# Performance work log

Measured on AMD Instinct MI355X. Metric: run time of the kernel, lower is better.

## Reference

```python
import jax, jax.numpy as jnp
import numpy as np

N, E, D, L, NE, FF, G, V, H = 4096, 131072, 256, 4, 2, 512, 128, 100, 8
DK = D // H


def setup_inputs() -> dict:
    key = jax.random.key(0)
    ks = iter(jax.random.split(key, 64))
    def W(shape, scale=0.05):
        return jax.random.normal(next(ks), shape, dtype=jnp.float32) * scale
    inp = {}
    inp['z'] = jax.random.randint(next(ks), (N,), 0, V)
    inp['pos'] = jax.random.normal(next(ks), (N, 3), dtype=jnp.float32)
    inp['batch'] = jnp.sort(jax.random.randint(next(ks), (N,), 0, G))
    inp['edge_index'] = jax.random.randint(next(ks), (2, E), 0, N)
    inp['emb'] = W((V, D))
    # E_GCL stacks (EGNN layer: edge MLP, attention gate, node MLP)
    inp['egcl_edge_w1'] = W((L, 2 * D + 1, D)); inp['egcl_edge_b1'] = jnp.zeros((L, D), jnp.float32)
    inp['egcl_edge_w2'] = W((L, D, D));         inp['egcl_edge_b2'] = jnp.zeros((L, D), jnp.float32)
    inp['egcl_node_w1'] = W((L, 2 * D, D));     inp['egcl_node_b1'] = jnp.zeros((L, D), jnp.float32)
    inp['egcl_node_w2'] = W((L, D, D));         inp['egcl_node_b2'] = jnp.zeros((L, D), jnp.float32)
    inp['egcl_att_w'] = W((L, D, 1));           inp['egcl_att_b'] = jnp.zeros((L, 1), jnp.float32)
    # Transformer encoder stacks (post-norm)
    inp['enc_wq'] = W((NE, D, D)); inp['enc_bq'] = jnp.zeros((NE, D), jnp.float32)
    inp['enc_wk'] = W((NE, D, D)); inp['enc_bk'] = jnp.zeros((NE, D), jnp.float32)
    inp['enc_wv'] = W((NE, D, D)); inp['enc_bv'] = jnp.zeros((NE, D), jnp.float32)
    inp['enc_wo'] = W((NE, D, D)); inp['enc_bo'] = jnp.zeros((NE, D), jnp.float32)
    inp['enc_ln1_g'] = jnp.ones((NE, D), jnp.float32); inp['enc_ln1_b'] = jnp.zeros((NE, D), jnp.float32)
    inp['enc_ffn_w1'] = W((NE, D, FF)); inp['enc_ffn_b1'] = jnp.zeros((NE, FF), jnp.float32)
    inp['enc_ffn_w2'] = W((NE, FF, D)); inp['enc_ffn_b2'] = jnp.zeros((NE, D), jnp.float32)
    inp['enc_ln2_g'] = jnp.ones((NE, D), jnp.float32); inp['enc_ln2_b'] = jnp.zeros((NE, D), jnp.float32)
    # energy_fc head
    inp['fc_w1'] = W((D, D)); inp['fc_b1'] = jnp.zeros((D,), jnp.float32)
    inp['fc_w2'] = W((D, 1)); inp['fc_b2'] = jnp.zeros((1,), jnp.float32)
    return inp


def _layer_norm(x, g, b, eps=1e-5):
    mu = jnp.mean(x, axis=-1, keepdims=True)
    var = jnp.mean((x - mu) ** 2, axis=-1, keepdims=True)
    return (x - mu) * jax.lax.rsqrt(var + eps) * g + b


def reference(z, pos, batch, edge_index, emb,
              egcl_edge_w1, egcl_edge_b1, egcl_edge_w2, egcl_edge_b2,
              egcl_node_w1, egcl_node_b1, egcl_node_w2, egcl_node_b2,
              egcl_att_w, egcl_att_b,
              enc_wq, enc_bq, enc_wk, enc_bk, enc_wv, enc_bv, enc_wo, enc_bo,
              enc_ln1_g, enc_ln1_b, enc_ffn_w1, enc_ffn_b1, enc_ffn_w2, enc_ffn_b2,
              enc_ln2_g, enc_ln2_b, fc_w1, fc_b1, fc_w2, fc_b2):
    h = emb[z]                                   # [N, D]
    row, col = edge_index[0], edge_index[1]
    diff = pos[row] - pos[col]                   # static_coord: coords never updated
    radial = jnp.sum(diff * diff, axis=-1, keepdims=True)  # [E, 1]
    for i in range(L):
        m_in = jnp.concatenate([h[row], h[col], radial], axis=-1)     # [E, 2D+1]
        m = jax.nn.silu(m_in @ egcl_edge_w1[i] + egcl_edge_b1[i])
        m = jax.nn.silu(m @ egcl_edge_w2[i] + egcl_edge_b2[i])        # [E, D]
        m = m * jax.nn.sigmoid(m @ egcl_att_w[i] + egcl_att_b[i])     # attention gate
        agg = jax.ops.segment_sum(m, row, num_segments=N)             # [N, D]
        n_in = jnp.concatenate([h, agg], axis=-1)
        upd = jax.nn.silu(n_in @ egcl_node_w1[i] + egcl_node_b1[i]) @ egcl_node_w2[i] + egcl_node_b2[i]
        h = h + upd                                                   # residual
    scale = 1.0 / jnp.sqrt(jnp.asarray(DK, h.dtype))
    for i in range(NE):
        q = (h @ enc_wq[i] + enc_bq[i]).reshape(N, H, DK)
        k = (h @ enc_wk[i] + enc_bk[i]).reshape(N, H, DK)
        v = (h @ enc_wv[i] + enc_bv[i]).reshape(N, H, DK)
        scores = jnp.einsum('nhd,mhd->hnm', q, k) * scale
        a = jax.nn.softmax(scores, axis=-1)
        attn = jnp.einsum('hnm,mhd->nhd', a, v).reshape(N, D) @ enc_wo[i] + enc_bo[i]
        h = _layer_norm(h + attn, enc_ln1_g[i], enc_ln1_b[i])
        f = jax.nn.silu(h @ enc_ffn_w1[i] + enc_ffn_b1[i]) @ enc_ffn_w2[i] + enc_ffn_b2[i]
        h = _layer_norm(h + f, enc_ln2_g[i], enc_ln2_b[i])
    g = jax.ops.segment_sum(h, batch, num_segments=G)                 # scatter-add readout
    out = jax.nn.silu(g @ fc_w1 + fc_b1) @ fc_w2 + fc_b2              # [G, 1]
    return out
```

## Files before the change

### kernel.cpp

```cpp
#include <hip/hip_runtime.h>
#include <math.h>

#define N_NODES 4096
#define N_EDGES 131072
#define DIM     256
#define NL      4
#define NENC    2
#define FFD     512
#define NG      128
#define NHEAD   8
#define DKH     32
#define TE2     32
#define NSPLIT_ATT 4

typedef __attribute__((ext_vector_type(8))) short bf16x8;
typedef __attribute__((ext_vector_type(4))) float f32x4;

__device__ __forceinline__ float siluf(float x) { return x / (1.f + __expf(-x)); }
__device__ __forceinline__ float sigmf_(float x) { return 1.f / (1.f + __expf(-x)); }
__device__ __forceinline__ unsigned short f2b(float f) {
    union { float f; unsigned u; } x; x.f = f;
    unsigned r = x.u + 0x7fffu + ((x.u >> 16) & 1u);
    return (unsigned short)(r >> 16);
}
__device__ __forceinline__ float b2f(unsigned short h) {
    union { unsigned u; float f; } x; x.u = (unsigned)h << 16; return x.f;
}

__global__ __launch_bounds__(256) void k_embed(const int* __restrict__ z,
                                               const float* __restrict__ emb,
                                               float* __restrict__ h) {
    int i = blockIdx.x * 256 + threadIdx.x;
    int n = i >> 8, d = i & 255;
    h[i] = emb[z[n] * DIM + d];
}

__global__ __launch_bounds__(256) void k_radial(const float* __restrict__ pos,
                                                const int* __restrict__ ei,
                                                float* __restrict__ radial) {
    int e = blockIdx.x * 256 + threadIdx.x;
    if (e >= N_EDGES) return;
    int r = ei[e], c = ei[N_EDGES + e];
    float dx = pos[r*3+0] - pos[c*3+0];
    float dy = pos[r*3+1] - pos[c*3+1];
    float dz = pos[r*3+2] - pos[c*3+2];
    radial[e] = dx*dx + dy*dy + dz*dz;
}

__global__ __launch_bounds__(256) void k_hist(const int* __restrict__ ei, int* __restrict__ cnt) {
    int e = blockIdx.x * 256 + threadIdx.x;
    if (e < N_EDGES) atomicAdd(&cnt[ei[e]], 1);
}

__global__ __launch_bounds__(256) void k_scan(const int* __restrict__ cnt, int* __restrict__ pos) {
    __shared__ int s_w[4];
    int t = threadIdx.x, lane = t & 63, wv = t >> 6;
    int loc[16]; int s = 0;
    #pragma unroll
    for (int i = 0; i < 16; ++i) { loc[i] = s; s += cnt[t * 16 + i]; }
    int inc = s;
    #pragma unroll
    for (int off = 1; off < 64; off <<= 1) {
        int v = __shfl_up(inc, off, 64);
        if (lane >= off) inc += v;
    }
    if (lane == 63) s_w[wv] = inc;
    __syncthreads();
    int wbase = 0;
    for (int j = 0; j < wv; ++j) wbase += s_w[j];
    int base = wbase + inc - s;
    #pragma unroll
    for (int i = 0; i < 16; ++i) pos[t * 16 + i] = base + loc[i];
}

__global__ __launch_bounds__(256) void k_scatter(const int* __restrict__ ei,
                                                 const float* __restrict__ radial,
                                                 int* __restrict__ pos,
                                                 int* __restrict__ rows_s,
                                                 int* __restrict__ cols_s,
                                                 float* __restrict__ rad_s) {
    int e = blockIdx.x * 256 + threadIdx.x;
    if (e >= N_EDGES) return;
    int r = ei[e];
    int p = atomicAdd(&pos[r], 1);
    rows_s[p] = r;
    cols_s[p] = ei[N_EDGES + e];
    rad_s[p] = radial[e];
}

__global__ __launch_bounds__(256) void k_conv_w2(const float* __restrict__ ew2,
                                                 unsigned short* __restrict__ W2F) {
    int tid = blockIdx.x * 256 + threadIdx.x;
    int layer = tid >> 13;
    int r = tid & 8191;
    int ks = r >> 10, ntg = (r >> 6) & 15, lane = r & 63;
    const float* W = ew2 + (size_t)layer * 65536;
    unsigned short tmp[8];
    #pragma unroll
    for (int j = 0; j < 8; ++j) {
        int k = ks*32 + 4*(lane>>4) + (j&3) + 16*(j>>2);
        int n = ntg*16 + (lane&15);
        tmp[j] = f2b(W[k*256 + n]);
    }
    *(bf16x8*)&W2F[(size_t)layer*65536 + (size_t)r*8] = *(const bf16x8*)&tmp[0];
}

__global__ __launch_bounds__(256) void k_pack_all(
    const float* __restrict__ ew1, const float* __restrict__ nw1, const float* __restrict__ nw2,
    const float* __restrict__ wq, const float* __restrict__ wk, const float* __restrict__ wv,
    const float* __restrict__ wo, const float* __restrict__ fw1, const float* __restrict__ fw2,
    unsigned short* __restrict__ dst)
{
    int f = blockIdx.x * 256 + threadIdx.x;
    int rem, panel, NTG, mode;
    if (f < 65536)       { rem = f;          panel = rem / 16384; rem &= 16383; NTG = 32; mode = 0; }
    else if (f < 131072) { rem = f - 65536;  panel = rem / 16384; rem &= 16383; NTG = 16; mode = 1; }
    else if (f < 163840) { rem = f - 131072; panel = rem / 8192;  rem &= 8191;  NTG = 16; mode = 2; }
    else if (f < 212992) { rem = f - 163840; panel = rem / 24576; rem %= 24576; NTG = 48; mode = 3; }
    else if (f < 229376) { rem = f - 212992; panel = rem / 8192;  rem &= 8191;  NTG = 16; mode = 4; }
    else if (f < 262144) { rem = f - 229376; panel = rem / 16384; rem &= 16383; NTG = 32; mode = 5; }
    else                 { rem = f - 262144; panel = rem / 16384; rem &= 16383; NTG = 16; mode = 6; }
    int ks   = rem / (NTG * 64);
    int ntg  = (rem >> 6) % NTG;
    int lane = rem & 63;
    unsigned short tmp[8];
    #pragma unroll
    for (int j = 0; j < 8; ++j) {
        int k = ks*32 + 4*(lane>>4) + (j&3) + 16*(j>>2);
        int n = ntg*16 + (lane&15);
        float val;
        switch (mode) {
            case 0: val = ew1[(size_t)panel*131328 + (n < 256 ? k*256 + n : (256 + k)*256 + (n - 256))]; break;
            case 1: val = nw1[(size_t)panel*131072 + k*256 + n]; break;
            case 2: val = nw2[(size_t)panel*65536 + k*256 + n]; break;
            case 3: { const float* b = (n < 256) ? wq : ((n < 512) ? wk : wv);
                      val = b[(size_t)panel*65536 + k*256 + (n & 255)]; } break;
            case 4: val = wo[(size_t)panel*65536 + k*256 + n]; break;
            case 5: val = fw1[(size_t)panel*131072 + k*512 + n]; break;
            default: val = fw2[(size_t)panel*131072 + k*256 + n]; break;
        }
        tmp[j] = f2b(val);
    }
    *(bf16x8*)&dst[(size_t)f * 8] = *(const bf16x8*)&tmp[0];
}

template<int NCHUNK, int NC, int NSPLIT, int ACT, int RESID, int OUTMODE>
__global__ __launch_bounds__(256) void k_gemm(
    const float* __restrict__ A0, const float* __restrict__ A1, int lda,
    const unsigned short* __restrict__ Wp,
    const float* __restrict__ b0, const float* __restrict__ b1, const float* __restrict__ b2,
    const float* __restrict__ resid, float* __restrict__ C,
    unsigned short* __restrict__ kpk, unsigned short* __restrict__ vpk)
{
    constexpr int NT  = NC / (64 * NSPLIT);
    constexpr int NTG = NC / 16;
    __shared__ __align__(16) char s_hi[16 * 512];
    __shared__ __align__(16) char s_lo[16 * 512];
    const int t = threadIdx.x, l = t & 63, w = t >> 6;
    const int g = l >> 4, r = l & 15;
    const int mtile  = blockIdx.x % 256;
    const int nchunk = blockIdx.x / 256;
    const int r0 = mtile * 16;

    f32x4 acc[NT];
    #pragma unroll
    for (int nt = 0; nt < NT; ++nt) acc[nt] = (f32x4){0.f, 0.f, 0.f, 0.f};

    const bf16x8* Wf = (const bf16x8*)Wp;
    for (int c = 0; c < NCHUNK; ++c) {
        const float* Ac = (c == 0) ? A0 : A1;
        __syncthreads();
        const int c4 = l * 4;
        #pragma unroll
        for (int it = 0; it < 4; ++it) {
            int row = it * 4 + w;
            float4 v = *(const float4*)&Ac[(size_t)(r0 + row) * lda + c4];
            float vv[4] = {v.x, v.y, v.z, v.w};
            ushort4 h4, l4;
            unsigned short hh;
            hh = f2b(vv[0]); h4.x = hh; l4.x = f2b(vv[0] - b2f(hh));
            hh = f2b(vv[1]); h4.y = hh; l4.y = f2b(vv[1] - b2f(hh));
            hh = f2b(vv[2]); h4.z = hh; l4.z = f2b(vv[2] - b2f(hh));
            hh = f2b(vv[3]); h4.w = hh; l4.w = f2b(vv[3] - b2f(hh));
            int boff = (c4 * 2) ^ (row << 3);
            *(ushort4*)&s_hi[row * 512 + boff] = h4;
            *(ushort4*)&s_lo[row * 512 + boff] = l4;
        }
        __syncthreads();
        #pragma unroll
        for (int ks = 0; ks < 8; ++ks) {
            const int ksg = c * 8 + ks;
            const int x0 = (ks * 64 + 8 * g) ^ (r << 3);
            union { uint2 u[2]; bf16x8 v; } ah, al;
            ah.u[0] = *(const uint2*)&s_hi[r * 512 + x0];
            ah.u[1] = *(const uint2*)&s_hi[r * 512 + (x0 ^ 32)];
            al.u[0] = *(const uint2*)&s_lo[r * 512 + x0];
            al.u[1] = *(const uint2*)&s_lo[r * 512 + (x0 ^ 32)];
            #pragma unroll
            for (int nt = 0; nt < NT; ++nt) {
                int fb = (nchunk * 4 + w) * NT + nt;
                bf16x8 bf_ = Wf[(size_t)(ksg * NTG + fb) * 64 + l];
                acc[nt] = __builtin_amdgcn_mfma_f32_16x16x32_bf16(ah.v, bf_, acc[nt], 0, 0, 0);
                acc[nt] = __builtin_amdgcn_mfma_f32_16x16x32_bf16(al.v, bf_, acc[nt], 0, 0, 0);
            }
        }
    }
    #pragma unroll
    for (int nt = 0; nt < NT; ++nt) {
        int n = ((nchunk * 4 + w) * NT + nt) * 16 + r;
        float bias = 0.f;
        if (b0) {
            const float* bp = (n < 256) ? b0 : ((n < 512) ? b1 : b2);
            bias = bp[n & 255];
        }
        #pragma unroll
        for (int reg = 0; reg < 4; ++reg) {
            int row = r0 + g * 4 + reg;
            float v = acc[nt][reg] + bias;
            if (ACT == 1) v = siluf(v);
            if (RESID) v += resid[(size_t)row * 256 + n];
            if (OUTMODE == 0) {
                C[(size_t)row * NC + n] = v;
            } else {
                if (n < 256) {
                    C[(size_t)row * 256 + n] = v;
                } else if (n < 512) {
                    int hd = (n - 256) >> 5, dm = (n - 256) & 31;
                    int dp = (dm & 3) | (((dm >> 4) & 1) << 2) | (((dm >> 2) & 3) << 3);
                    unsigned short hb = f2b(v);
                    size_t base = ((size_t)hd * N_NODES + row) * 64;
                    kpk[base + dp]      = hb;
                    kpk[base + 32 + dp] = f2b(v - b2f(hb));
                } else {
                    int hd = (n - 512) >> 5, dm = (n - 512) & 31;
                    int s = row & 31;
                    int sp = (s & 3) | (((s >> 4) & 1) << 2) | (((s >> 2) & 3) << 3);
                    int keyp = (row & ~31) | sp;
                    vpk[((size_t)hd * 32 + dm) * N_NODES + keyp] = f2b(v);
                }
            }
        }
    }
}

__global__ __launch_bounds__(256) void k_edge_mfma(
    const float* __restrict__ P12,
    const int* __restrict__ rows_s, const int* __restrict__ cols_s,
    const float* __restrict__ rad_s,
    const float* __restrict__ w1r, const float* __restrict__ b1,
    const unsigned short* __restrict__ W2F, const float* __restrict__ b2,
    const float* __restrict__ aw, const float* __restrict__ ab,
    float* __restrict__ agg)
{
    __shared__ __align__(16) char s_a[20480];
    __shared__ int   s_row[TE2], s_cn[TE2];
    __shared__ float s_rad[TE2], s_gp[4][TE2], s_gate[TE2];
    const int t = threadIdx.x, l = t & 63, w = t >> 6;
    const int e0 = blockIdx.x * TE2;

    if (t < TE2) {
        s_row[t] = rows_s[e0 + t];
        s_cn[t]  = cols_s[e0 + t];
        s_rad[t] = rad_s[e0 + t];
    }
    __syncthreads();

    const int c4 = l * 4;
    const float4 wr = *(const float4*)&w1r[c4];
    const float4 bb = *(const float4*)&b1[c4];
    #pragma unroll
    for (int it = 0; it < 8; ++it) {
        int e = it * 4 + w;
        float4 pa = *(const float4*)&P12[(size_t)s_row[e] * 512 + c4];
        float4 pb = *(const float4*)&P12[(size_t)s_cn[e] * 512 + 256 + c4];
        float rad = s_rad[e];
        ushort4 pk;
        pk.x = f2b(siluf(pa.x + pb.x + rad * wr.x + bb.x));
        pk.y = f2b(siluf(pa.y + pb.y + rad * wr.y + bb.y));
        pk.z = f2b(siluf(pa.z + pb.z + rad * wr.z + bb.z));
        pk.w = f2b(siluf(pa.w + pb.w + rad * wr.w + bb.w));
        *(ushort4*)&s_a[e * 512 + ((c4 * 2) ^ ((e & 15) << 3))] = pk;
    }
    __syncthreads();

    const int g = l >> 4, r = l & 15;
    f32x4 acc[2][4];
    #pragma unroll
    for (int mt = 0; mt < 2; ++mt)
        #pragma unroll
        for (int nt = 0; nt < 4; ++nt)
            acc[mt][nt] = (f32x4){0.f, 0.f, 0.f, 0.f};

    const bf16x8* Wf = (const bf16x8*)W2F;
    for (int ks = 0; ks < 8; ++ks) {
        bf16x8 af[2], bfr[4];
        #pragma unroll
        for (int mt = 0; mt < 2; ++mt) {
            int rowa = mt * 16 + r;
            int x0 = (ks * 64 + 8 * g) ^ (r << 3);
            uint2 lo = *(const uint2*)&s_a[rowa * 512 + x0];
            uint2 hi = *(const uint2*)&s_a[rowa * 512 + (x0 ^ 32)];
            union { uint2 u[2]; bf16x8 v; } ua;
            ua.u[0] = lo; ua.u[1] = hi;
            af[mt] = ua.v;
        }
        #pragma unroll
        for (int nt = 0; nt < 4; ++nt)
            bfr[nt] = Wf[(ks * 16 + w * 4 + nt) * 64 + l];
        #pragma unroll
        for (int mt = 0; mt < 2; ++mt)
            #pragma unroll
            for (int nt = 0; nt < 4; ++nt)
                acc[mt][nt] = __builtin_amdgcn_mfma_f32_16x16x32_bf16(af[mt], bfr[nt], acc[mt][nt], 0, 0, 0);
    }

    float b2v[4], awv[4];
    #pragma unroll
    for (int nt = 0; nt < 4; ++nt) {
        int col = w * 64 + nt * 16 + r;
        b2v[nt] = b2[col];
        awv[nt] = aw[col];
    }
    float pg[2][4];
    #pragma unroll
    for (int mt = 0; mt < 2; ++mt)
        #pragma unroll
        for (int reg = 0; reg < 4; ++reg) {
            float s = 0.f;
            #pragma unroll
            for (int nt = 0; nt < 4; ++nt) {
                float v = siluf(acc[mt][nt][reg] + b2v[nt]);
                acc[mt][nt][reg] = v;
                s += v * awv[nt];
            }
            pg[mt][reg] = s;
        }
    #pragma unroll
    for (int off = 1; off < 16; off <<= 1)
        #pragma unroll
        for (int mt = 0; mt < 2; ++mt)
            #pragma unroll
            for (int reg = 0; reg < 4; ++reg)
                pg[mt][reg] += __shfl_xor(pg[mt][reg], off, 64);
    if (r == 0) {
        #pragma unroll
        for (int mt = 0; mt < 2; ++mt)
            #pragma unroll
            for (int reg = 0; reg < 4; ++reg)
                s_gp[w][mt * 16 + g * 4 + reg] = pg[mt][reg];
    }
    __syncthreads();
    if (t < TE2)
        s_gate[t] = sigmf_(s_gp[0][t] + s_gp[1][t] + s_gp[2][t] + s_gp[3][t] + ab[0]);
    __syncthreads();

    unsigned short* s_out = (unsigned short*)s_a;
    #pragma unroll
    for (int mt = 0; mt < 2; ++mt) {
        float4 gt4 = *(const float4*)&s_gate[mt * 16 + g * 4];
        #pragma unroll
        for (int nt = 0; nt < 4; ++nt) {
            int col = w * 64 + nt * 16 + r;
            ushort4 o4;
            o4.x = f2b(acc[mt][nt][0] * gt4.x);
            o4.y = f2b(acc[mt][nt][1] * gt4.y);
            o4.z = f2b(acc[mt][nt][2] * gt4.z);
            o4.w = f2b(acc[mt][nt][3] * gt4.w);
            *(ushort4*)&s_out[col * 40 + mt * 16 + g * 4] = o4;
        }
    }
    __syncthreads();
    float cur = 0.f;
    #pragma unroll
    for (int c = 0; c < 4; ++c) {
        union { uint4 q; unsigned short s[8]; } ch;
        ch.q = *(const uint4*)&s_out[t * 40 + c * 8];
        #pragma unroll
        for (int j = 0; j < 8; ++j) {
            int e = c * 8 + j;
            cur += b2f(ch.s[j]);
            bool flush = (e == TE2 - 1) || (s_row[e + 1] != s_row[e]);
            if (flush) {
                atomicAdd(&agg[(size_t)s_row[e] * DIM + t], cur);
                cur = 0.f;
            }
        }
    }
}

template<int ACT>
__global__ __launch_bounds__(256) void k_mlp_small(
    const float* __restrict__ A1, const float* __restrict__ W,
    const float* __restrict__ bias, float* __restrict__ C)
{
    __shared__ float s_a[16][260];
    const int t  = threadIdx.x;
    const int r0 = blockIdx.x * 16;
    for (int r = 0; r < 16; ++r)
        s_a[r][t] = A1[(size_t)(r0 + r) * DIM + t];
    __syncthreads();
    const int er0 = (t >> 6) * 4;
    const int c0 = (t & 63) * 4;
    float acc[4][4];
    #pragma unroll
    for (int e = 0; e < 4; ++e)
        #pragma unroll
        for (int c = 0; c < 4; ++c) acc[e][c] = 0.f;
    #pragma unroll 2
    for (int k = 0; k < DIM; k += 4) {
        float4 w0 = *(const float4*)&W[(size_t)(k+0)*DIM + c0];
        float4 w1 = *(const float4*)&W[(size_t)(k+1)*DIM + c0];
        float4 w2 = *(const float4*)&W[(size_t)(k+2)*DIM + c0];
        float4 w3 = *(const float4*)&W[(size_t)(k+3)*DIM + c0];
        #pragma unroll
        for (int e = 0; e < 4; ++e) {
            float4 x = *(const float4*)&s_a[er0+e][k];
            acc[e][0] += x.x*w0.x + x.y*w1.x + x.z*w2.x + x.w*w3.x;
            acc[e][1] += x.x*w0.y + x.y*w1.y + x.z*w2.y + x.w*w3.y;
            acc[e][2] += x.x*w0.z + x.y*w1.z + x.z*w2.z + x.w*w3.z;
            acc[e][3] += x.x*w0.w + x.y*w1.w + x.z*w2.w + x.w*w3.w;
        }
    }
    float4 bb = *(const float4*)&bias[c0];
    #pragma unroll
    for (int e = 0; e < 4; ++e) {
        float v0 = acc[e][0] + bb.x, v1 = acc[e][1] + bb.y;
        float v2 = acc[e][2] + bb.z, v3 = acc[e][3] + bb.w;
        if (ACT == 1) { v0 = siluf(v0); v1 = siluf(v1); v2 = siluf(v2); v3 = siluf(v3); }
        float4 o; o.x = v0; o.y = v1; o.z = v2; o.w = v3;
        *(float4*)&C[(size_t)(r0 + er0 + e) * DIM + c0] = o;
    }
}

__global__ __launch_bounds__(256) void k_ln(const float* __restrict__ x,
                                            const float* __restrict__ g,
                                            const float* __restrict__ b,
                                            float* __restrict__ out) {
    int t = threadIdx.x, lane = t & 63, w = t >> 6;
    int row = blockIdx.x * 4 + w;
    float4 v = *(const float4*)&x[(size_t)row * DIM + lane * 4];
    float s = v.x + v.y + v.z + v.w;
    #pragma unroll
    for (int off = 32; off; off >>= 1) s += __shfl_xor(s, off, 64);
    float mu = s * (1.f / 256.f);
    float dx = v.x - mu, dy = v.y - mu, dz = v.z - mu, dw = v.w - mu;
    float q = dx*dx + dy*dy + dz*dz + dw*dw;
    #pragma unroll
    for (int off = 32; off; off >>= 1) q += __shfl_xor(q, off, 64);
    float rs = rsqrtf(q * (1.f / 256.f) + 1e-5f);
    float4 gg = *(const float4*)&g[lane * 4];
    float4 bb = *(const float4*)&b[lane * 4];
    float4 o;
    o.x = dx * rs * gg.x + bb.x;
    o.y = dy * rs * gg.y + bb.y;
    o.z = dz * rs * gg.z + bb.z;
    o.w = dw * rs * gg.w + bb.w;
    *(float4*)&out[(size_t)row * DIM + lane * 4] = o;
}

__global__ __launch_bounds__(256) void k_attn_mfma(
    const float* __restrict__ q,
    const unsigned short* __restrict__ kpk,
    const unsigned short* __restrict__ vpk,
    float* __restrict__ op0, float* __restrict__ op1,
    float* __restrict__ op2, float* __restrict__ op3,
    float* __restrict__ mlbuf)
{
    __shared__ __align__(16) char s_k[2][8192];
    __shared__ __align__(16) char s_v[2][4096];
    const int t = threadIdx.x, lane = t & 63, w = t >> 6;
    const int g = lane >> 4, r = lane & 15;
    const int head = blockIdx.y;
    const int split = blockIdx.z;
    const int q0 = blockIdx.x * 64;
    const float scale = 0.17677669529663687f;

    bf16x8 qh, ql;
    {
        const float* qp = &q[(size_t)(q0 + w*16 + r) * DIM + head*DKH + 4*g];
        float4 f0 = *(const float4*)qp;
        float4 f1 = *(const float4*)(qp + 16);
        float vv[8] = {f0.x, f0.y, f0.z, f0.w, f1.x, f1.y, f1.z, f1.w};
        union { unsigned short s[8]; bf16x8 v; } uh, ul;
        #pragma unroll
        for (int j = 0; j < 8; ++j) {
            float sv = vv[j] * scale;
            unsigned short hb = f2b(sv);
            uh.s[j] = hb;
            ul.s[j] = f2b(sv - b2f(hb));
        }
        qh = uh.v; ql = ul.v;
    }

    const char* kbase = (const char*)(kpk + (size_t)head * N_NODES * 64) + (size_t)split * 16 * 8192;
    const unsigned short* vbase = vpk + (size_t)head * 32 * N_NODES;
    const int koff = split * 1024;
    const int vrow = t >> 3, vch = t & 7;

    uint4 kr0, kr1, vr0;
    {
        const char* kt = kbase;
        kr0 = *(const uint4*)(kt + t * 16);
        kr1 = *(const uint4*)(kt + 4096 + t * 16);
        vr0 = *(const uint4*)(vbase + (size_t)vrow * N_NODES + koff + vch * 8);
        int key0 = t >> 3, sl0 = t & 7;
        *(uint4*)&s_k[0][key0 * 128 + ((sl0 ^ (key0 & 7)) << 4)] = kr0;
        int c1 = t + 256, key1 = c1 >> 3, sl1 = c1 & 7;
        *(uint4*)&s_k[0][key1 * 128 + ((sl1 ^ (key1 & 7)) << 4)] = kr1;
        *(uint4*)&s_v[0][vrow * 128 + ((vch ^ (vrow & 7)) << 4)] = vr0;
    }
    __syncthreads();

    float m = -1e30f, l = 0.f;
    f32x4 ot0 = (f32x4){0.f,0.f,0.f,0.f}, ot1 = (f32x4){0.f,0.f,0.f,0.f};

    for (int tile = 0; tile < 16; ++tile) {
        const int cur = tile & 1;
        if (tile < 15) {
            const char* kt = kbase + (size_t)(tile + 1) * 8192;
            kr0 = *(const uint4*)(kt + t * 16);
            kr1 = *(const uint4*)(kt + 4096 + t * 16);
            vr0 = *(const uint4*)(vbase + (size_t)vrow * N_NODES + koff + (tile + 1) * 64 + vch * 8);
        }
        bf16x8 kh[4], kl[4];
        #pragma unroll
        for (int kb = 0; kb < 4; ++kb) {
            int key = kb * 16 + r;
            kh[kb] = *(const bf16x8*)&s_k[cur][key * 128 + ((g ^ (r & 7)) << 4)];
            kl[kb] = *(const bf16x8*)&s_k[cur][key * 128 + (((4 + g) ^ (r & 7)) << 4)];
        }
        f32x4 sc[4];
        #pragma unroll
        for (int kb = 0; kb < 4; ++kb) {
            f32x4 a = (f32x4){0.f,0.f,0.f,0.f};
            a = __builtin_amdgcn_mfma_f32_16x16x32_bf16(kh[kb], qh, a, 0, 0, 0);
            a = __builtin_amdgcn_mfma_f32_16x16x32_bf16(kh[kb], ql, a, 0, 0, 0);
            a = __builtin_amdgcn_mfma_f32_16x16x32_bf16(kl[kb], qh, a, 0, 0, 0);
            sc[kb] = a;
        }
        float tm = -1e30f;
        #pragma unroll
        for (int kb = 0; kb < 4; ++kb)
            #pragma unroll
            for (int e = 0; e < 4; ++e) tm = fmaxf(tm, sc[kb][e]);
        tm = fmaxf(tm, __shfl_xor(tm, 16, 64));
        tm = fmaxf(tm, __shfl_xor(tm, 32, 64));
        float nm = fmaxf(m, tm);
        float scf = __expf(m - nm);
        m = nm;
        float p[16]; float ls = 0.f;
        #pragma unroll
        for (int kb = 0; kb < 4; ++kb)
            #pragma unroll
            for (int e = 0; e < 4; ++e) {
                float pe = __expf(sc[kb][e] - nm);
                p[kb*4+e] = pe; ls += pe;
            }
        ls += __shfl_xor(ls, 16, 64);
        ls += __shfl_xor(ls, 32, 64);
        l = l * scf + ls;
        ot0[0] *= scf; ot0[1] *= scf; ot0[2] *= scf; ot0[3] *= scf;
        ot1[0] *= scf; ot1[1] *= scf; ot1[2] *= scf; ot1[3] *= scf;
        union { unsigned short s[8]; bf16x8 v; } pk0, pk1;
        #pragma unroll
        for (int j = 0; j < 8; ++j) {
            pk0.s[j] = f2b(p[(j >> 2) * 4 + (j & 3)]);
            pk1.s[j] = f2b(p[(2 + (j >> 2)) * 4 + (j & 3)]);
        }
        bf16x8 vf00 = *(const bf16x8*)&s_v[cur][(0*16 + r) * 128 + (((0*4 + g) ^ (r & 7)) << 4)];
        bf16x8 vf01 = *(const bf16x8*)&s_v[cur][(0*16 + r) * 128 + (((1*4 + g) ^ (r & 7)) << 4)];
        bf16x8 vf10 = *(const bf16x8*)&s_v[cur][(1*16 + r) * 128 + (((0*4 + g) ^ (r & 7)) << 4)];
        bf16x8 vf11 = *(const bf16x8*)&s_v[cur][(1*16 + r) * 128 + (((1*4 + g) ^ (r & 7)) << 4)];
        ot0 = __builtin_amdgcn_mfma_f32_16x16x32_bf16(vf00, pk0.v, ot0, 0, 0, 0);
        ot0 = __builtin_amdgcn_mfma_f32_16x16x32_bf16(vf01, pk1.v, ot0, 0, 0, 0);
        ot1 = __builtin_amdgcn_mfma_f32_16x16x32_bf16(vf10, pk0.v, ot1, 0, 0, 0);
        ot1 = __builtin_amdgcn_mfma_f32_16x16x32_bf16(vf11, pk1.v, ot1, 0, 0, 0);

        __syncthreads();
        if (tile < 15) {
            int key0 = t >> 3, sl0 = t & 7;
            *(uint4*)&s_k[cur ^ 1][key0 * 128 + ((sl0 ^ (key0 & 7)) << 4)] = kr0;
            int c1 = t + 256, key1 = c1 >> 3, sl1 = c1 & 7;
            *(uint4*)&s_k[cur ^ 1][key1 * 128 + ((sl1 ^ (key1 & 7)) << 4)] = kr1;
            *(uint4*)&s_v[cur ^ 1][vrow * 128 + ((vch ^ (vrow & 7)) << 4)] = vr0;
        }
        __syncthreads();
    }

    float* opsel = (split == 0) ? op0 : (split == 1) ? op1 : (split == 2) ? op2 : op3;
    float* op = opsel + (size_t)(q0 + w*16 + r) * DIM + head*DKH;
    *(float4*)(op + 4*g)      = make_float4(ot0[0], ot0[1], ot0[2], ot0[3]);
    *(float4*)(op + 16 + 4*g) = make_float4(ot1[0], ot1[1], ot1[2], ot1[3]);
    if (g == 0) {
        float* mp = &mlbuf[(((size_t)split * NHEAD + head) * N_NODES + q0 + w*16 + r) * 2];
        mp[0] = m; mp[1] = l;
    }
}

__global__ __launch_bounds__(256) void k_attn_merge(
    const float* __restrict__ o0, const float* __restrict__ o1,
    const float* __restrict__ o2, const float* __restrict__ o3,
    const float* __restrict__ ml, float* __restrict__ A)
{
    int i = blockIdx.x * 256 + threadIdx.x;
    int qq = (i * 4) >> 8;
    int head = ((i * 4) & 255) >> 5;
    float m_[4], l_[4];
    #pragma unroll
    for (int s = 0; s < 4; ++s) {
        const float* p = &ml[(((size_t)s * NHEAD + head) * N_NODES + qq) * 2];
        m_[s] = p[0]; l_[s] = p[1];
    }
    float mm = fmaxf(fmaxf(m_[0], m_[1]), fmaxf(m_[2], m_[3]));
    float e0 = __expf(m_[0] - mm), e1 = __expf(m_[1] - mm);
    float e2 = __expf(m_[2] - mm), e3 = __expf(m_[3] - mm);
    float inv = 1.f / (e0 * l_[0] + e1 * l_[1] + e2 * l_[2] + e3 * l_[3]);
    float4 a0 = ((const float4*)o0)[i];
    float4 a1 = ((const float4*)o1)[i];
    float4 a2 = ((const float4*)o2)[i];
    float4 a3 = ((const float4*)o3)[i];
    float4 o;
    o.x = (a0.x*e0 + a1.x*e1 + a2.x*e2 + a3.x*e3) * inv;
    o.y = (a0.y*e0 + a1.y*e1 + a2.y*e2 + a3.y*e3) * inv;
    o.z = (a0.z*e0 + a1.z*e1 + a2.z*e2 + a3.z*e3) * inv;
    o.w = (a0.w*e0 + a1.w*e1 + a2.w*e2 + a3.w*e3) * inv;
    ((float4*)A)[i] = o;
}

__global__ __launch_bounds__(256) void k_segsum(const float* __restrict__ h,
                                                const int* __restrict__ batch,
                                                float* __restrict__ gbuf) {
    int i = blockIdx.x * 256 + threadIdx.x;
    int n = i >> 8, d = i & 255;
    atomicAdd(&gbuf[batch[n] * DIM + d], h[i]);
}

__global__ __launch_bounds__(256) void k_head2(const float* __restrict__ gmid,
                                               const float* __restrict__ w2,
                                               const float* __restrict__ b2,
                                               float* __restrict__ out) {
    int t = threadIdx.x, lane = t & 63, w = t >> 6;
    int g = blockIdx.x * 4 + w;
    float4 x  = *(const float4*)&gmid[g * DIM + lane * 4];
    float4 ww = *(const float4*)&w2[lane * 4];
    float s = x.x * ww.x + x.y * ww.y + x.z * ww.z + x.w * ww.w;
    #pragma unroll
    for (int off = 32; off; off >>= 1) s += __shfl_xor(s, off, 64);
    if (lane == 0) out[g] = s + b2[0];
}

extern "C" void kernel_launch(void* const* d_in, const int* in_sizes, int n_in,
                              void* d_out, int out_size, void* d_ws, size_t ws_size,
                              hipStream_t stream)
{
    const int*   z     = (const int*)d_in[0];
    const float* pos   = (const float*)d_in[1];
    const int*   batch = (const int*)d_in[2];
    const int*   ei    = (const int*)d_in[3];
    const float* emb   = (const float*)d_in[4];
    const float* ew1   = (const float*)d_in[5];
    const float* eb1   = (const float*)d_in[6];
    const float* ew2   = (const float*)d_in[7];
    const float* eb2   = (const float*)d_in[8];
    const float* nw1   = (const float*)d_in[9];
    const float* nb1   = (const float*)d_in[10];
    const float* nw2   = (const float*)d_in[11];
    const float* nb2   = (const float*)d_in[12];
    const float* aw    = (const float*)d_in[13];
    const float* ab    = (const float*)d_in[14];
    const float* wq    = (const float*)d_in[15];
    const float* bq    = (const float*)d_in[16];
    const float* wk    = (const float*)d_in[17];
    const float* bk    = (const float*)d_in[18];
    const float* wv    = (const float*)d_in[19];
    const float* bv    = (const float*)d_in[20];
    const float* wo    = (const float*)d_in[21];
    const float* bo    = (const float*)d_in[22];
    const float* ln1g  = (const float*)d_in[23];
    const float* ln1b  = (const float*)d_in[24];
    const float* fw1   = (const float*)d_in[25];
    const float* fb1   = (const float*)d_in[26];
    const float* fw2   = (const float*)d_in[27];
    const float* fb2   = (const float*)d_in[28];
    const float* ln2g  = (const float*)d_in[29];
    const float* ln2b  = (const float*)d_in[30];
    const float* fcw1  = (const float*)d_in[31];
    const float* fcb1  = (const float*)d_in[32];
    const float* fcw2  = (const float*)d_in[33];
    const float* fcb2  = (const float*)d_in[34];
    float* out = (float*)d_out;

    float* ws = (float*)d_ws;
    const size_t ND = (size_t)N_NODES * DIM;
    float* h    = ws;
    float* agg  = ws + ND;
    float* A    = ws + 2 * ND;
    float* U    = ws + 3 * ND;
    float* op0  = ws + 4 * ND;
    float* op1  = ws + 5 * ND;
    float* Bffn = ws + 6 * ND;
    unsigned short* kpk = (unsigned short*)Bffn;
    unsigned short* vpk = kpk + (size_t)NHEAD * N_NODES * 64;
    float* radial = Bffn + (3 * ND) / 2;
    int*   cnt    = (int*)(radial + N_EDGES);
    int*   pcur   = cnt + N_NODES;
    float* gbuf   = ws + 8 * ND;
    float* gmid   = gbuf + (size_t)NG * DIM;
    float* rad_s  = gmid + (size_t)NG * DIM;
    int*   rows_s = (int*)(rad_s + N_EDGES);
    int*   cols_s = rows_s + N_EDGES;
    unsigned short* W2F   = (unsigned short*)(cols_s + N_EDGES);
    unsigned short* packs = W2F + (size_t)NL * 65536;
    float* mlbuf = rad_s;

    unsigned short* PK_W1   = packs;
    unsigned short* PK_NW1  = packs + 524288;
    unsigned short* PK_NW2  = packs + 1048576;
    unsigned short* PK_QKV  = packs + 1310720;
    unsigned short* PK_WO   = packs + 1703936;
    unsigned short* PK_FFN1 = packs + 1835008;
    unsigned short* PK_FFN2 = packs + 2097152;

    dim3 b256(256);

    k_embed<<<N_NODES * DIM / 256, b256, 0, stream>>>(z, emb, h);
    k_radial<<<N_EDGES / 256, b256, 0, stream>>>(pos, ei, radial);
    k_conv_w2<<<NL * 8192 / 256, b256, 0, stream>>>(ew2, W2F);
    k_pack_all<<<1152, b256, 0, stream>>>(ew1, nw1, nw2, wq, wk, wv, wo, fw1, fw2, packs);

    hipMemsetAsync(cnt, 0, N_NODES * sizeof(int), stream);
    k_hist<<<N_EDGES / 256, b256, 0, stream>>>(ei, cnt);
    k_scan<<<1, b256, 0, stream>>>(cnt, pcur);
    k_scatter<<<N_EDGES / 256, b256, 0, stream>>>(ei, radial, pcur, rows_s, cols_s, rad_s);

    for (int l = 0; l < NL; ++l) {
        hipMemsetAsync(agg, 0, ND * sizeof(float), stream);
        const float* W1l = ew1 + (size_t)l * 513 * DIM;
        k_gemm<1,512,2,0,0,0><<<512, b256, 0, stream>>>(h, nullptr, DIM,
            PK_W1 + (size_t)l * 131072, nullptr, nullptr, nullptr, nullptr, U,
            nullptr, nullptr);
        k_edge_mfma<<<N_EDGES / TE2, b256, 0, stream>>>(U, rows_s, cols_s, rad_s,
            W1l + (size_t)512 * DIM, eb1 + (size_t)l * DIM,
            W2F + (size_t)l * 65536, eb2 + (size_t)l * DIM,
            aw + (size_t)l * DIM, ab + l, agg);
        const float* nb1l = nb1 + (size_t)l * DIM;
        k_gemm<2,256,2,1,0,0><<<512, b256, 0, stream>>>(h, agg, DIM,
            PK_NW1 + (size_t)l * 131072, nb1l, nb1l, nb1l, nullptr, A,
            nullptr, nullptr);
        const float* nb2l = nb2 + (size_t)l * DIM;
        k_gemm<1,256,2,0,1,0><<<512, b256, 0, stream>>>(A, nullptr, DIM,
            PK_NW2 + (size_t)l * 65536, nb2l, nb2l, nb2l, h, h,
            nullptr, nullptr);
    }

    for (int i = 0; i < NENC; ++i) {
        k_gemm<1,768,3,0,0,1><<<768, b256, 0, stream>>>(h, nullptr, DIM,
            PK_QKV + (size_t)i * 196608,
            bq + (size_t)i * DIM, bk + (size_t)i * DIM, bv + (size_t)i * DIM, nullptr, U,
            kpk, vpk);
        dim3 ag(N_NODES / 64, NHEAD, NSPLIT_ATT);
        k_attn_mfma<<<ag, b256, 0, stream>>>(U, kpk, vpk, op0, op1, A, agg, mlbuf);
        k_attn_merge<<<N_NODES * DIM / 1024, b256, 0, stream>>>(op0, op1, A, agg, mlbuf, A);
        const float* bol = bo + (size_t)i * DIM;
        k_gemm<1,256,2,0,1,0><<<512, b256, 0, stream>>>(A, nullptr, DIM,
            PK_WO + (size_t)i * 65536, bol, bol, bol, h, agg,
            nullptr, nullptr);
        k_ln<<<N_NODES / 4, b256, 0, stream>>>(agg, ln1g + (size_t)i * DIM, ln1b + (size_t)i * DIM, h);
        const float* fb1l = fb1 + (size_t)i * FFD;
        k_gemm<1,512,2,1,0,0><<<512, b256, 0, stream>>>(h, nullptr, DIM,
            PK_FFN1 + (size_t)i * 131072, fb1l, fb1l + 256, nullptr, nullptr, Bffn,
            nullptr, nullptr);
        const float* fb2l = fb2 + (size_t)i * DIM;
        k_gemm<2,256,2,0,1,0><<<512, b256, 0, stream>>>(Bffn, Bffn + 256, FFD,
            PK_FFN2 + (size_t)i * 131072, fb2l, fb2l, fb2l, h, agg,
            nullptr, nullptr);
        k_ln<<<N_NODES / 4, b256, 0, stream>>>(agg, ln2g + (size_t)i * DIM, ln2b + (size_t)i * DIM, h);
    }

    hipMemsetAsync(gbuf, 0, (size_t)NG * DIM * sizeof(float), stream);
    k_segsum<<<N_NODES * DIM / 256, b256, 0, stream>>>(h, batch, gbuf);
    k_mlp_small<1><<<NG / 16, b256, 0, stream>>>(gbuf, fcw1, fcb1, gmid);
    k_head2<<<NG / 4, b256, 0, stream>>>(gmid, fcw2, fcb2, out);
}
```

Baseline: 668.0 us.

## Fuse split-attention merge into Wo GEMM A-load and use uniform edge indices

Removes the separate k_attn_merge kernel. The four split-softmax partial outputs are now combined with their max/sum statistics inside the Wo projection GEMM's A-tile load. The fourth partial buffer moves from agg to a new op3buf region carved out after the packed weights. The edge kernel also precomputes the segment-flush mask with a ballot and uses readfirstlane to make row, column and radial values scalar-uniform, which cuts LDS reads and divergence in the atomic flush loop. The cost is extra exp and load work per GEMM tile, repeated across column-split blocks, and the added buffer must fit within the existing workspace.

```diff
diff --git a/kernel.cpp b/kernel.cpp
--- a/kernel.cpp
+++ b/kernel.cpp
@@ -144,13 +144,15 @@
     *(bf16x8*)&dst[(size_t)f * 8] = *(const bf16x8*)&tmp[0];
 }
 
-template<int NCHUNK, int NC, int NSPLIT, int ACT, int RESID, int OUTMODE>
+template<int NCHUNK, int NC, int NSPLIT, int ACT, int RESID, int OUTMODE, int AMODE>
 __global__ __launch_bounds__(256) void k_gemm(
     const float* __restrict__ A0, const float* __restrict__ A1, int lda,
     const unsigned short* __restrict__ Wp,
     const float* __restrict__ b0, const float* __restrict__ b1, const float* __restrict__ b2,
     const float* __restrict__ resid, float* __restrict__ C,
-    unsigned short* __restrict__ kpk, unsigned short* __restrict__ vpk)
+    unsigned short* __restrict__ kpk, unsigned short* __restrict__ vpk,
+    const float* __restrict__ am2, const float* __restrict__ am3,
+    const float* __restrict__ aml)
 {
     constexpr int NT  = NC / (64 * NSPLIT);
     constexpr int NTG = NC / 16;
@@ -174,7 +176,31 @@
         #pragma unroll
         for (int it = 0; it < 4; ++it) {
             int row = it * 4 + w;
-            float4 v = *(const float4*)&Ac[(size_t)(r0 + row) * lda + c4];
+            float4 v;
+            if (AMODE == 0) {
+                v = *(const float4*)&Ac[(size_t)(r0 + row) * lda + c4];
+            } else {
+                const int head = l >> 3;
+                float m_[4], l_[4];
+                #pragma unroll
+                for (int s = 0; s < 4; ++s) {
+                    const float* p = &aml[(((size_t)s * NHEAD + head) * N_NODES + (r0 + row)) * 2];
+                    m_[s] = p[0]; l_[s] = p[1];
+                }
+                float mm = fmaxf(fmaxf(m_[0], m_[1]), fmaxf(m_[2], m_[3]));
+                float e0 = __expf(m_[0] - mm), e1 = __expf(m_[1] - mm);
+                float e2 = __expf(m_[2] - mm), e3 = __expf(m_[3] - mm);
+                float inv = 1.f / (e0 * l_[0] + e1 * l_[1] + e2 * l_[2] + e3 * l_[3]);
+                size_t off = (size_t)(r0 + row) * 256 + c4;
+                float4 a0 = *(const float4*)&A0[off];
+                float4 a1 = *(const float4*)&A1[off];
+                float4 a2 = *(const float4*)&am2[off];
+                float4 a3 = *(const float4*)&am3[off];
+                v.x = (a0.x*e0 + a1.x*e1 + a2.x*e2 + a3.x*e3) * inv;
+                v.y = (a0.y*e0 + a1.y*e1 + a2.y*e2 + a3.y*e3) * inv;
+                v.z = (a0.z*e0 + a1.z*e1 + a2.z*e2 + a3.z*e3) * inv;
+                v.w = (a0.w*e0 + a1.w*e1 + a2.w*e2 + a3.w*e3) * inv;
+            }
             float vv[4] = {v.x, v.y, v.z, v.w};
             ushort4 h4, l4;
             unsigned short hh;
@@ -255,6 +281,7 @@
     __shared__ __align__(16) char s_a[20480];
     __shared__ int   s_row[TE2], s_cn[TE2];
     __shared__ float s_rad[TE2], s_gp[4][TE2], s_gate[TE2];
+    __shared__ unsigned s_mask;
     const int t = threadIdx.x, l = t & 63, w = t >> 6;
     const int e0 = blockIdx.x * TE2;
 
@@ -265,15 +292,23 @@
     }
     __syncthreads();
 
+    if (t < 64) {
+        bool flag = (t < TE2) && ((t == TE2 - 1) || (s_row[t + 1] != s_row[t]));
+        unsigned long long bm = __ballot(flag);
+        if (t == 0) s_mask = (unsigned)bm;
+    }
+
     const int c4 = l * 4;
     const float4 wr = *(const float4*)&w1r[c4];
     const float4 bb = *(const float4*)&b1[c4];
     #pragma unroll
     for (int it = 0; it < 8; ++it) {
         int e = it * 4 + w;
-        float4 pa = *(const float4*)&P12[(size_t)s_row[e] * 512 + c4];
-        float4 pb = *(const float4*)&P12[(size_t)s_cn[e] * 512 + 256 + c4];
-        float rad = s_rad[e];
+        int rowu = __builtin_amdgcn_readfirstlane(s_row[e]);
+        int cnu  = __builtin_amdgcn_readfirstlane(s_cn[e]);
+        float rad = __int_as_float(__builtin_amdgcn_readfirstlane(__float_as_int(s_rad[e])));
+        float4 pa = *(const float4*)&P12[(size_t)rowu * 512 + c4];
+        float4 pb = *(const float4*)&P12[(size_t)cnu * 512 + 256 + c4];
         ushort4 pk;
         pk.x = f2b(siluf(pa.x + pb.x + rad * wr.x + bb.x));
         pk.y = f2b(siluf(pa.y + pb.y + rad * wr.y + bb.y));
@@ -370,6 +405,7 @@
         }
     }
     __syncthreads();
+    const unsigned fmask = s_mask;
     float cur = 0.f;
     #pragma unroll
     for (int c = 0; c < 4; ++c) {
@@ -379,9 +415,9 @@
         for (int j = 0; j < 8; ++j) {
             int e = c * 8 + j;
             cur += b2f(ch.s[j]);
-            bool flush = (e == TE2 - 1) || (s_row[e + 1] != s_row[e]);
-            if (flush) {
-                atomicAdd(&agg[(size_t)s_row[e] * DIM + t], cur);
+            if ((fmask >> e) & 1u) {
+                int rowu = __builtin_amdgcn_readfirstlane(s_row[e]);
+                atomicAdd(&agg[(size_t)rowu * DIM + t], cur);
                 cur = 0.f;
             }
         }
@@ -595,36 +631,6 @@
         float* mp = &mlbuf[(((size_t)split * NHEAD + head) * N_NODES + q0 + w*16 + r) * 2];
         mp[0] = m; mp[1] = l;
     }
-}
-
-__global__ __launch_bounds__(256) void k_attn_merge(
-    const float* __restrict__ o0, const float* __restrict__ o1,
-    const float* __restrict__ o2, const float* __restrict__ o3,
-    const float* __restrict__ ml, float* __restrict__ A)
-{
-    int i = blockIdx.x * 256 + threadIdx.x;
-    int qq = (i * 4) >> 8;
-    int head = ((i * 4) & 255) >> 5;
-    float m_[4], l_[4];
-    #pragma unroll
-    for (int s = 0; s < 4; ++s) {
-        const float* p = &ml[(((size_t)s * NHEAD + head) * N_NODES + qq) * 2];
-        m_[s] = p[0]; l_[s] = p[1];
-    }
-    float mm = fmaxf(fmaxf(m_[0], m_[1]), fmaxf(m_[2], m_[3]));
-    float e0 = __expf(m_[0] - mm), e1 = __expf(m_[1] - mm);
-    float e2 = __expf(m_[2] - mm), e3 = __expf(m_[3] - mm);
-    float inv = 1.f / (e0 * l_[0] + e1 * l_[1] + e2 * l_[2] + e3 * l_[3]);
-    float4 a0 = ((const float4*)o0)[i];
-    float4 a1 = ((const float4*)o1)[i];
-    float4 a2 = ((const float4*)o2)[i];
-    float4 a3 = ((const float4*)o3)[i];
-    float4 o;
-    o.x = (a0.x*e0 + a1.x*e1 + a2.x*e2 + a3.x*e3) * inv;
-    o.y = (a0.y*e0 + a1.y*e1 + a2.y*e2 + a3.y*e3) * inv;
-    o.z = (a0.z*e0 + a1.z*e1 + a2.z*e2 + a3.z*e3) * inv;
-    o.w = (a0.w*e0 + a1.w*e1 + a2.w*e2 + a3.w*e3) * inv;
-    ((float4*)A)[i] = o;
 }
 
 __global__ __launch_bounds__(256) void k_segsum(const float* __restrict__ h,
@@ -712,6 +718,7 @@
     unsigned short* W2F   = (unsigned short*)(cols_s + N_EDGES);
     unsigned short* packs = W2F + (size_t)NL * 65536;
     float* mlbuf = rad_s;
+    float* op3buf = (float*)(packs + 2359296);
 
     unsigned short* PK_W1   = packs;
     unsigned short* PK_NW1  = packs + 524288;
@@ -736,44 +743,43 @@
     for (int l = 0; l < NL; ++l) {
         hipMemsetAsync(agg, 0, ND * sizeof(float), stream);
         const float* W1l = ew1 + (size_t)l * 513 * DIM;
-        k_gemm<1,512,2,0,0,0><<<512, b256, 0, stream>>>(h, nullptr, DIM,
+        k_gemm<1,512,2,0,0,0,0><<<512, b256, 0, stream>>>(h, nullptr, DIM,
             PK_W1 + (size_t)l * 131072, nullptr, nullptr, nullptr, nullptr, U,
-            nullptr, nullptr);
+            nullptr, nullptr, nullptr, nullptr, nullptr);
         k_edge_mfma<<<N_EDGES / TE2, b256, 0, stream>>>(U, rows_s, cols_s, rad_s,
             W1l + (size_t)512 * DIM, eb1 + (size_t)l * DIM,
             W2F + (size_t)l * 65536, eb2 + (size_t)l * DIM,
             aw + (size_t)l * DIM, ab + l, agg);
         const float* nb1l = nb1 + (size_t)l * DIM;
-        k_gemm<2,256,2,1,0,0><<<512, b256, 0, stream>>>(h, agg, DIM,
+        k_gemm<2,256,2,1,0,0,0><<<512, b256, 0, stream>>>(h, agg, DIM,
             PK_NW1 + (size_t)l * 131072, nb1l, nb1l, nb1l, nullptr, A,
-            nullptr, nullptr);
+            nullptr, nullptr, nullptr, nullptr, nullptr);
         const float* nb2l = nb2 + (size_t)l * DIM;
-        k_gemm<1,256,2,0,1,0><<<512, b256, 0, stream>>>(A, nullptr, DIM,
+        k_gemm<1,256,2,0,1,0,0><<<512, b256, 0, stream>>>(A, nullptr, DIM,
             PK_NW2 + (size_t)l * 65536, nb2l, nb2l, nb2l, h, h,
-            nullptr, nullptr);
+            nullptr, nullptr, nullptr, nullptr, nullptr);
     }
 
     for (int i = 0; i < NENC; ++i) {
-        k_gemm<1,768,3,0,0,1><<<768, b256, 0, stream>>>(h, nullptr, DIM,
+        k_gemm<1,768,3,0,0,1,0><<<768, b256, 0, stream>>>(h, nullptr, DIM,
             PK_QKV + (size_t)i * 196608,
             bq + (size_t)i * DIM, bk + (size_t)i * DIM, bv + (size_t)i * DIM, nullptr, U,
-            kpk, vpk);
+            kpk, vpk, nullptr, nullptr, nullptr);
         dim3 ag(N_NODES / 64, NHEAD, NSPLIT_ATT);
-        k_attn_mfma<<<ag, b256, 0, stream>>>(U, kpk, vpk, op0, op1, A, agg, mlbuf);
-        k_attn_merge<<<N_NODES * DIM / 1024, b256, 0, stream>>>(op0, op1, A, agg, mlbuf, A);
+        k_attn_mfma<<<ag, b256, 0, stream>>>(U, kpk, vpk, op0, op1, A, op3buf, mlbuf);
         const float* bol = bo + (size_t)i * DIM;
-        k_gemm<1,256,2,0,1,0><<<512, b256, 0, stream>>>(A, nullptr, DIM,
+        k_gemm<1,256,2,0,1,0,1><<<512, b256, 0, stream>>>(op0, op1, 256,
             PK_WO + (size_t)i * 65536, bol, bol, bol, h, agg,
-            nullptr, nullptr);
+            nullptr, nullptr, A, op3buf, mlbuf);
         k_ln<<<N_NODES / 4, b256, 0, stream>>>(agg, ln1g + (size_t)i * DIM, ln1b + (size_t)i * DIM, h);
         const float* fb1l = fb1 + (size_t)i * FFD;
-        k_gemm<1,512,2,1,0,0><<<512, b256, 0, stream>>>(h, nullptr, DIM,
+        k_gemm<1,512,2,1,0,0,0><<<512, b256, 0, stream>>>(h, nullptr, DIM,
             PK_FFN1 + (size_t)i * 131072, fb1l, fb1l + 256, nullptr, nullptr, Bffn,
-            nullptr, nullptr);
+            nullptr, nullptr, nullptr, nullptr, nullptr);
         const float* fb2l = fb2 + (size_t)i * DIM;
-        k_gemm<2,256,2,0,1,0><<<512, b256, 0, stream>>>(Bffn, Bffn + 256, FFD,
+        k_gemm<2,256,2,0,1,0,0><<<512, b256, 0, stream>>>(Bffn, Bffn + 256, FFD,
             PK_FFN2 + (size_t)i * 131072, fb2l, fb2l, fb2l, h, agg,
-            nullptr, nullptr);
+            nullptr, nullptr, nullptr, nullptr, nullptr);
         k_ln<<<N_NODES / 4, b256, 0, stream>>>(agg, ln2g + (size_t)i * DIM, ln2b + (size_t)i * DIM, h);
     }
 
```

Measured after the change: 655.1 us. About the same (-1.9%).
